# Performance work log

Measured on AMD Instinct MI355X. Metric: run time of the kernel, lower is better.

## Reference

```python
import jax, jax.numpy as jnp
import numpy as np

EMBED = 512
HEADS = 8
HEAD_DIM = EMBED // HEADS


def setup_inputs() -> dict:
    key = jax.random.key(0)
    ks = jax.random.split(key, 12)
    B, L, D = 2, 4096, EMBED
    s = 1.0 / np.sqrt(D)  # torch Linear default init range scale (approx, uniform)
    def lin(k):
        kw, kb = jax.random.split(k)
        W = jax.random.uniform(kw, (D, D), jnp.float32, -s, s)
        b = jax.random.uniform(kb, (D,), jnp.float32, -s, s)
        return W, b
    Wq, bq = lin(ks[0])
    Wk, bk = lin(ks[1])
    Wv, bv = lin(ks[2])
    Wo, bo = lin(ks[3])
    query = jax.random.normal(ks[4], (B, L, D), jnp.float32)
    key_t = jax.random.normal(ks[5], (B, L, D), jnp.float32)
    value = jax.random.normal(ks[6], (B, L, D), jnp.float32)
    return {"query": query, "key": key_t, "value": value,
            "Wq": Wq, "bq": bq, "Wk": Wk, "bk": bk,
            "Wv": Wv, "bv": bv, "Wo": Wo, "bo": bo}


def reference(query, key, value, Wq, bq, Wk, bk, Wv, bv, Wo, bo):
    B, L, D = query.shape
    H, Hd = HEADS, HEAD_DIM
    scale = Hd ** -0.5
    # torch nn.Linear: y = x @ W.T + b
    q = (query @ Wq.T + bq).reshape(B, L, H, Hd).transpose(0, 2, 1, 3)   # [B,H,L,Hd]
    k = (key   @ Wk.T + bk).reshape(B, -1, H, Hd).transpose(0, 2, 1, 3)
    v = (value @ Wv.T + bv).reshape(B, -1, H, Hd).transpose(0, 2, 1, 3)
    scores = jnp.einsum('bhqd,bhkd->bhqk', q, k) * scale                  # [B,H,L,L]
    causal = jnp.triu(jnp.ones((L, L), dtype=bool), k=1)                  # True above diag
    neg = jnp.finfo(scores.dtype).min
    scores = jnp.where(causal, neg, scores)
    attn = jax.nn.softmax(scores, axis=-1)
    # dropout is identity in eval mode
    out = jnp.einsum('bhqk,bhkd->bhqd', attn, v)                          # [B,H,L,Hd]
    out = out.transpose(0, 2, 1, 3).reshape(B, L, D)
    return out @ Wo.T + bo, attn
```

## Files before the change

### kernel.cpp

```cpp
#include <hip/hip_runtime.h>
#include <hip/hip_bf16.h>


typedef __attribute__((ext_vector_type(8))) __bf16 bf16x8;
typedef __attribute__((ext_vector_type(4))) __bf16 bf16v4;
typedef __attribute__((ext_vector_type(4))) float f32x4;

constexpr int LL = 4096;
constexpr int DD = 512;
constexpr int HH = 8;
constexpr int HD = 64;
constexpr int BB = 2;
constexpr int BL = BB * LL;
constexpr size_t OUT_ELEMS = (size_t)BB * LL * DD;
constexpr int CH = 8;
constexpr int NCHUNK = LL / 64 / CH;
constexpr int CHUNKS_PER_BH = 288;

static __device__ inline int chunk_off(int qb) {
    const int g = qb >> 3, r = qb & 7;
    return qb + 4 * g * (g - 1) + r * g;
}

static __device__ inline bf16x8 cvt8(const float* p) {
    float4 a = *reinterpret_cast<const float4*>(p);
    float4 b = *reinterpret_cast<const float4*>(p + 4);
    bf16x8 r;
    r[0] = (__bf16)a.x; r[1] = (__bf16)a.y; r[2] = (__bf16)a.z; r[3] = (__bf16)a.w;
    r[4] = (__bf16)b.x; r[5] = (__bf16)b.y; r[6] = (__bf16)b.z; r[7] = (__bf16)b.w;
    return r;
}

__global__ __launch_bounds__(256) void cvt_kernel(
    const float* __restrict__ q, const float* __restrict__ k,
    const float* __restrict__ v, __bf16* __restrict__ o)
{
    constexpr size_t N = (size_t)BL * DD;
    size_t i = ((size_t)blockIdx.x * 256 + threadIdx.x) * 8;
    const float* src = q; size_t j = i;
    if (i >= 2 * N)      { src = v; j = i - 2 * N; }
    else if (i >= N)     { src = k; j = i - N; }
    *reinterpret_cast<bf16x8*>(&o[i]) = cvt8(&src[j]);
}

__global__ __launch_bounds__(256) void qkv_kernel(
    const __bf16* __restrict__ Xb,
    const float* __restrict__ Wq, const float* __restrict__ bq,
    const float* __restrict__ Wk, const float* __restrict__ bk,
    const float* __restrict__ Wv, const float* __restrict__ bv,
    __bf16* __restrict__ Qb, __bf16* __restrict__ Kb, __bf16* __restrict__ Vt)
{
    const int z = blockIdx.z;
    const __bf16* x  = Xb + (size_t)z * BL * DD;
    const float* W   = (z == 0) ? Wq : (z == 1) ? Wk : Wv;
    const float* bia = (z == 0) ? bq : (z == 1) ? bk : bv;

    const int wid = threadIdx.x >> 6;
    const int lane = threadIdx.x & 63;
    const int l15 = lane & 15;
    const int lg  = lane >> 4;

    const int r0 = blockIdx.x * 64;
    const int cb = blockIdx.y;
    const int c0 = cb * 64 + wid * 16;

    f32x4 acc[4] = {};
    for (int k0 = 0; k0 < DD; k0 += 32) {
        bf16x8 bfrag = cvt8(&W[(size_t)(c0 + l15) * DD + k0 + lg * 8]);
#pragma unroll
        for (int mt = 0; mt < 4; ++mt) {
            bf16x8 afrag = *reinterpret_cast<const bf16x8*>(
                &x[(size_t)(r0 + mt * 16 + l15) * DD + k0 + lg * 8]);
            acc[mt] = __builtin_amdgcn_mfma_f32_16x16x32_bf16(afrag, bfrag, acc[mt], 0, 0, 0);
        }
    }

    __shared__ __bf16 T[64][72];
    const float bval = bia[c0 + l15];
#pragma unroll
    for (int mt = 0; mt < 4; ++mt)
#pragma unroll
        for (int i = 0; i < 4; ++i) {
            const float val = acc[mt][i] + bval;
            const int row = mt * 16 + lg * 4 + i;
            const int col = wid * 16 + l15;
            if (z == 2) T[col][row] = (__bf16)val;
            else        T[row][col] = (__bf16)val;
        }
    __syncthreads();

    const int tr  = threadIdx.x >> 2;
    const int seg = threadIdx.x & 3;
    uint4 v0 = *reinterpret_cast<const uint4*>(&T[tr][seg * 16]);
    uint4 v1 = *reinterpret_cast<const uint4*>(&T[tr][seg * 16 + 8]);
    const int b  = r0 >> 12;
    const int l0 = r0 & (LL - 1);
    if (z == 2) {
        __bf16* dst = Vt + ((size_t)(b * HH + cb) * HD + tr) * LL + l0 + seg * 16;
        *reinterpret_cast<uint4*>(dst)     = v0;
        *reinterpret_cast<uint4*>(dst + 8) = v1;
    } else {
        __bf16* base = (z == 0) ? Qb : Kb;
        __bf16* dst = base + ((size_t)(b * HH + cb) * LL + l0 + tr) * HD + seg * 16;
        *reinterpret_cast<uint4*>(dst)     = v0;
        *reinterpret_cast<uint4*>(dst + 8) = v1;
    }
}

__global__ __launch_bounds__(256, 4) void rowsum_kernel(
    const __bf16* __restrict__ Qb, const __bf16* __restrict__ Kb,
    float* __restrict__ rspart)
{
    const int bh = blockIdx.x;
    const int qb = 63 - blockIdx.y;
    const int ch = blockIdx.z;
    const int kb0 = ch * CH;
    if (kb0 > qb) return;

    const int wv   = threadIdx.x >> 6;
    const int lane = threadIdx.x & 63;
    const int l15  = lane & 15;
    const int lg   = lane >> 4;

    const __bf16* Qh = Qb + (size_t)bh * LL * HD;
    const __bf16* Kh = Kb + (size_t)bh * LL * HD;

    const int q0 = qb * 64 + wv * 16;
    const int qrow = q0 + l15;
    const bf16x8 qf0 = *reinterpret_cast<const bf16x8*>(&Qh[(size_t)qrow * HD + lg * 8]);
    const bf16x8 qf1 = *reinterpret_cast<const bf16x8*>(&Qh[(size_t)qrow * HD + 32 + lg * 8]);
    const float SC = 0.125f * 1.44269504088896f;

    auto loadK = [&](bf16x8 (&kf)[8], int kb) {
        const __bf16* kp = &Kh[((size_t)kb * 64 + l15) * HD + lg * 8];
#pragma unroll
        for (int kt = 0; kt < 4; ++kt) {
            kf[kt * 2]     = *reinterpret_cast<const bf16x8*>(kp + (size_t)kt * 16 * HD);
            kf[kt * 2 + 1] = *reinterpret_cast<const bf16x8*>(kp + (size_t)kt * 16 * HD + 32);
        }
    };

    float rs = 0.f;
    auto body = [&](bf16x8 (&kf)[8], int kb) {
        f32x4 s[4] = {};
#pragma unroll
        for (int kt = 0; kt < 4; ++kt) {
            s[kt] = __builtin_amdgcn_mfma_f32_16x16x32_bf16(kf[kt * 2],     qf0, s[kt], 0, 0, 0);
            s[kt] = __builtin_amdgcn_mfma_f32_16x16x32_bf16(kf[kt * 2 + 1], qf1, s[kt], 0, 0, 0);
        }
        const bool diag = (kb == qb);
#pragma unroll
        for (int kt = 0; kt < 4; ++kt)
#pragma unroll
            for (int i = 0; i < 4; ++i) {
                float e = exp2f(s[kt][i] * SC);
                if (diag && (kb * 64 + kt * 16 + lg * 4 + i) > qrow) e = 0.f;
                rs += e;
            }
    };

    const int kend = (qb < kb0 + CH - 1) ? qb : kb0 + CH - 1;
    {
        bf16x8 kA[8], kB[8];
        int kb = kb0;
        bool useA = true;
        loadK(kA, kb);
        for (; kb <= kend; ++kb) {
            if (useA) { if (kb + 1 <= kend) loadK(kB, kb + 1); body(kA, kb); }
            else      { if (kb + 1 <= kend) loadK(kA, kb + 1); body(kB, kb); }
            useA = !useA;
        }
    }
    rs += __shfl_xor(rs, 16, 64);
    rs += __shfl_xor(rs, 32, 64);
    if (lane < 16)
        rspart[((size_t)bh * LL + qrow) * NCHUNK + ch] = rs;
}

__global__ __launch_bounds__(256, 3) void attn_main_kernel(
    const __bf16* __restrict__ Qb, const __bf16* __restrict__ Kb,
    const __bf16* __restrict__ Vt, const float* __restrict__ rspart,
    __bf16* __restrict__ opart, float* __restrict__ attn_out)
{
    const int bh = blockIdx.x;
    const int qb = 63 - blockIdx.y;
    const int ch = blockIdx.z;

    const int wv   = threadIdx.x >> 6;
    const int lane = threadIdx.x & 63;
    const int l15  = lane & 15;
    const int lg   = lane >> 4;

    float* A_out = attn_out + (size_t)bh * LL * LL;
    const int q0 = qb * 64 + wv * 16;
    const int qrow = q0 + l15;
    const int kb0 = ch * CH;

    const int srow = lane >> 4;
    const int scol = (lane & 15) * 4;

    auto zstore = [&](int kb) {
        const float4 z4 = {0.f, 0.f, 0.f, 0.f};
#pragma unroll
        for (int mt = 0; mt < 4; ++mt)
            *reinterpret_cast<float4*>(
                &A_out[(size_t)(q0 + mt * 4 + srow) * LL + kb * 64 + scol]) = z4;
    };

    if (kb0 > qb) {
        for (int t = 0; t < CH; ++t) zstore(kb0 + t);
        return;
    }

    const __bf16* Qh = Qb + (size_t)bh * LL * HD;
    const __bf16* Kh = Kb + (size_t)bh * LL * HD;
    const __bf16* Vh = Vt + (size_t)bh * HD * LL;

    __shared__ __bf16 P[4][16][72];

    const bf16x8 qf0 = *reinterpret_cast<const bf16x8*>(&Qh[(size_t)qrow * HD + lg * 8]);
    const bf16x8 qf1 = *reinterpret_cast<const bf16x8*>(&Qh[(size_t)qrow * HD + 32 + lg * 8]);

    float rsv = 0.f;
    const int nc = qb >> 3;
    const float* rp = &rspart[((size_t)bh * LL + qrow) * NCHUNK];
    for (int c = 0; c <= nc; ++c) rsv += rp[c];
    const float llog = -log2f(rsv);
    const float SC = 0.125f * 1.44269504088896f;

    f32x4 oacc[4] = {};

    auto loadK = [&](bf16x8 (&kf)[8], int kb) {
        const __bf16* kp = &Kh[((size_t)kb * 64 + l15) * HD + lg * 8];
#pragma unroll
        for (int kt = 0; kt < 4; ++kt) {
            kf[kt * 2]     = *reinterpret_cast<const bf16x8*>(kp + (size_t)kt * 16 * HD);
            kf[kt * 2 + 1] = *reinterpret_cast<const bf16x8*>(kp + (size_t)kt * 16 * HD + 32);
        }
    };

    auto body = [&](bf16x8 (&kf)[8], int kb) {
        bf16x8 vf[8];
        {
            const __bf16* vp = &Vh[(size_t)l15 * LL + (size_t)kb * 64 + lg * 8];
#pragma unroll
            for (int ht = 0; ht < 4; ++ht) {
                vf[ht * 2]     = *reinterpret_cast<const bf16x8*>(vp + (size_t)ht * 16 * LL);
                vf[ht * 2 + 1] = *reinterpret_cast<const bf16x8*>(vp + (size_t)ht * 16 * LL + 32);
            }
        }
        f32x4 s[4] = {};
#pragma unroll
        for (int kt = 0; kt < 4; ++kt) {
            s[kt] = __builtin_amdgcn_mfma_f32_16x16x32_bf16(kf[kt * 2],     qf0, s[kt], 0, 0, 0);
            s[kt] = __builtin_amdgcn_mfma_f32_16x16x32_bf16(kf[kt * 2 + 1], qf1, s[kt], 0, 0, 0);
        }
        const bool diag = (kb == qb);
#pragma unroll
        for (int kt = 0; kt < 4; ++kt) {
            float e0 = exp2f(fmaf(s[kt][0], SC, llog));
            float e1 = exp2f(fmaf(s[kt][1], SC, llog));
            float e2 = exp2f(fmaf(s[kt][2], SC, llog));
            float e3 = exp2f(fmaf(s[kt][3], SC, llog));
            if (diag) {
                const int kc = kb * 64 + kt * 16 + lg * 4;
                if (kc + 0 > qrow) e0 = 0.f;
                if (kc + 1 > qrow) e1 = 0.f;
                if (kc + 2 > qrow) e2 = 0.f;
                if (kc + 3 > qrow) e3 = 0.f;
            }
            float4 ev = {e0, e1, e2, e3};
            *reinterpret_cast<float4*>(
                &A_out[(size_t)qrow * LL + kb * 64 + kt * 16 + lg * 4]) = ev;
            bf16v4 pk;
            pk[0] = (__bf16)e0; pk[1] = (__bf16)e1;
            pk[2] = (__bf16)e2; pk[3] = (__bf16)e3;
            *reinterpret_cast<bf16v4*>(&P[wv][l15][kt * 16 + lg * 4]) = pk;
        }
        const bf16x8 pa0 = *reinterpret_cast<const bf16x8*>(&P[wv][l15][lg * 8]);
        const bf16x8 pa1 = *reinterpret_cast<const bf16x8*>(&P[wv][l15][32 + lg * 8]);
#pragma unroll
        for (int ht = 0; ht < 4; ++ht) {
            oacc[ht] = __builtin_amdgcn_mfma_f32_16x16x32_bf16(pa0, vf[ht * 2],     oacc[ht], 0, 0, 0);
            oacc[ht] = __builtin_amdgcn_mfma_f32_16x16x32_bf16(pa1, vf[ht * 2 + 1], oacc[ht], 0, 0, 0);
        }
    };

    const int kend = (qb < kb0 + CH - 1) ? qb : kb0 + CH - 1;
    {
        bf16x8 kA[8], kB[8];
        int kb = kb0;
        bool useA = true;
        loadK(kA, kb);
        for (; kb <= kend; ++kb) {
            if (useA) { if (kb + 1 <= kend) loadK(kB, kb + 1); body(kA, kb); }
            else      { if (kb + 1 <= kend) loadK(kA, kb + 1); body(kB, kb); }
            useA = !useA;
        }
    }
    for (int kb = qb + 1; kb < kb0 + CH; ++kb) zstore(kb);

#pragma unroll
    for (int ht = 0; ht < 4; ++ht)
#pragma unroll
        for (int i = 0; i < 4; ++i)
            P[wv][lg * 4 + i][ht * 16 + l15] = (__bf16)oacc[ht][i];
    const int arow = lane >> 2;
    const int aseg = lane & 3;
    uint4 o0 = *reinterpret_cast<const uint4*>(&P[wv][arow][aseg * 16]);
    uint4 o1 = *reinterpret_cast<const uint4*>(&P[wv][arow][aseg * 16 + 8]);
    __bf16* dst = opart
        + ((size_t)(bh * CHUNKS_PER_BH + chunk_off(qb) + ch)) * 4096
        + (wv * 16 + arow) * 64 + aseg * 16;
    *reinterpret_cast<uint4*>(dst)     = o0;
    *reinterpret_cast<uint4*>(dst + 8) = o1;
}

__global__ __launch_bounds__(256) void oreduce_kernel(
    const __bf16* __restrict__ opart, __bf16* __restrict__ Ob)
{
    const int bh = blockIdx.x;
    const int qb = blockIdx.y;
    const int nc = qb >> 3;
    const __bf16* src = opart + ((size_t)(bh * CHUNKS_PER_BH + chunk_off(qb))) * 4096;
    const int t = threadIdx.x;

    float acc[16] = {};
    for (int c = 0; c <= nc; ++c) {
        bf16x8 a = *reinterpret_cast<const bf16x8*>(&src[(size_t)c * 4096 + t * 16]);
        bf16x8 b = *reinterpret_cast<const bf16x8*>(&src[(size_t)c * 4096 + t * 16 + 8]);
#pragma unroll
        for (int j = 0; j < 8; ++j) { acc[j] += (float)a[j]; acc[8 + j] += (float)b[j]; }
    }
    bf16x8 r0, r1;
#pragma unroll
    for (int j = 0; j < 8; ++j) { r0[j] = (__bf16)acc[j]; r1[j] = (__bf16)acc[8 + j]; }

    const int qr  = t >> 2;
    const int hd0 = (t & 3) * 16;
    const int b = bh >> 3, h = bh & 7;
    __bf16* dst = Ob + ((size_t)(b * LL + qb * 64 + qr)) * DD + h * HD + hd0;
    *reinterpret_cast<bf16x8*>(dst)     = r0;
    *reinterpret_cast<bf16x8*>(dst + 8) = r1;
}

__global__ __launch_bounds__(256) void oproj_kernel(
    const __bf16* __restrict__ Ob, const float* __restrict__ Wo,
    const float* __restrict__ bo, float* __restrict__ out)
{
    const int wid = threadIdx.x >> 6;
    const int lane = threadIdx.x & 63;
    const int l15 = lane & 15;
    const int lg  = lane >> 4;

    const int r0 = blockIdx.x * 64;
    const int c0 = blockIdx.y * 64 + wid * 16;

    f32x4 acc[4] = {};
    for (int k0 = 0; k0 < DD; k0 += 32) {
        bf16x8 bfrag = cvt8(&Wo[(size_t)(c0 + l15) * DD + k0 + lg * 8]);
#pragma unroll
        for (int mt = 0; mt < 4; ++mt) {
            bf16x8 afrag = *reinterpret_cast<const bf16x8*>(
                &Ob[(size_t)(r0 + mt * 16 + l15) * DD + k0 + lg * 8]);
            acc[mt] = __builtin_amdgcn_mfma_f32_16x16x32_bf16(afrag, bfrag, acc[mt], 0, 0, 0);
        }
    }
    const float bval = bo[c0 + l15];
#pragma unroll
    for (int mt = 0; mt < 4; ++mt)
#pragma unroll
        for (int i = 0; i < 4; ++i)
            out[(size_t)(r0 + mt * 16 + lg * 4 + i) * DD + c0 + l15] = acc[mt][i] + bval;
}

extern "C" void kernel_launch(void* const* d_in, const int* in_sizes, int n_in,
                              void* d_out, int out_size, void* d_ws, size_t ws_size,
                              hipStream_t stream) {
    const float* query = (const float*)d_in[0];
    const float* key_t = (const float*)d_in[1];
    const float* value = (const float*)d_in[2];
    const float* Wq = (const float*)d_in[3];
    const float* bq = (const float*)d_in[4];
    const float* Wk = (const float*)d_in[5];
    const float* bk = (const float*)d_in[6];
    const float* Wv = (const float*)d_in[7];
    const float* bv = (const float*)d_in[8];
    const float* Wo = (const float*)d_in[9];
    const float* bo = (const float*)d_in[10];

    float* out  = (float*)d_out;
    float* attn = out + OUT_ELEMS;

    char* ws = (char*)d_ws;
    __bf16* Qb     = (__bf16*)(ws);
    __bf16* Kb     = (__bf16*)(ws +  8388608);
    __bf16* Vt     = (__bf16*)(ws + 16777216);
    __bf16* Ob     = (__bf16*)(ws + 25165824);
    float*  rspart = (float*) (ws + 33554432);
    __bf16* Xb     = (__bf16*)(ws + 35651584);
    __bf16* opart  = (__bf16*)(ws + 35651584);

    cvt_kernel<<<dim3(3 * BL * DD / 8 / 256), 256, 0, stream>>>(query, key_t, value, Xb);
    qkv_kernel<<<dim3(BL / 64, DD / 64, 3), 256, 0, stream>>>(
        Xb, Wq, bq, Wk, bk, Wv, bv, Qb, Kb, Vt);
    rowsum_kernel<<<dim3(BB * HH, LL / 64, NCHUNK), 256, 0, stream>>>(Qb, Kb, rspart);
    attn_main_kernel<<<dim3(BB * HH, LL / 64, NCHUNK), 256, 0, stream>>>(
        Qb, Kb, Vt, rspart, opart, attn);
    oreduce_kernel<<<dim3(BB * HH, LL / 64), 256, 0, stream>>>(opart, Ob);
    oproj_kernel<<<dim3(BL / 64, DD / 64), 256, 0, stream>>>(Ob, Wo, bo, out);
}
```

Before: 813.2 us.

## Move causal-zero fill to dedicated kernel and coalesce attn stores via LDS

The upper-triangle zero fill of the attention-probability output moves out of the attention kernel into a separate zero_kernel that writes contiguous row strips per query block. In the attention kernel, probabilities are first staged through a shared float tile so each wave writes full 64-float row segments instead of scattered 16-byte pieces. Both changes aim at better-coalesced HBM writes for the large attn tensor. The cost is an extra kernel launch and more shared memory (about 17KB more per block), which may reduce occupancy.

```diff
diff --git a/kernel.cpp b/kernel.cpp
--- a/kernel.cpp
+++ b/kernel.cpp
@@ -41,6 +41,27 @@
     if (i >= 2 * N)      { src = v; j = i - 2 * N; }
     else if (i >= N)     { src = k; j = i - N; }
     *reinterpret_cast<bf16x8*>(&o[i]) = cvt8(&src[j]);
+}
+
+__global__ __launch_bounds__(256) void zero_kernel(float* __restrict__ attn_out)
+{
+    const int bh = blockIdx.x;
+    const int qb = blockIdx.y;
+    const int z  = blockIdx.z;
+
+    const int wv   = threadIdx.x >> 6;
+    const int lane = threadIdx.x & 63;
+
+    const int strip = 1024 - (qb + 1) * 16;
+    const int col0  = (qb + 1) * 64 + z * strip;
+    float* base = attn_out + (size_t)bh * LL * LL + (size_t)qb * 64 * LL;
+
+    const f32x4 z4 = {0.f, 0.f, 0.f, 0.f};
+    for (int r = wv; r < 64; r += 4) {
+        float* row = base + (size_t)r * LL + col0;
+        for (int c = lane * 4; c < strip; c += 256)
+            *reinterpret_cast<f32x4*>(row + c) = z4;
+    }
 }
 
 __global__ __launch_bounds__(256) void qkv_kernel(
@@ -185,6 +206,8 @@
     const int bh = blockIdx.x;
     const int qb = 63 - blockIdx.y;
     const int ch = blockIdx.z;
+    const int kb0 = ch * CH;
+    if (kb0 > qb) return;
 
     const int wv   = threadIdx.x >> 6;
     const int lane = threadIdx.x & 63;
@@ -194,29 +217,13 @@
     float* A_out = attn_out + (size_t)bh * LL * LL;
     const int q0 = qb * 64 + wv * 16;
     const int qrow = q0 + l15;
-    const int kb0 = ch * CH;
-
-    const int srow = lane >> 4;
-    const int scol = (lane & 15) * 4;
-
-    auto zstore = [&](int kb) {
-        const float4 z4 = {0.f, 0.f, 0.f, 0.f};
-#pragma unroll
-        for (int mt = 0; mt < 4; ++mt)
-            *reinterpret_cast<float4*>(
-                &A_out[(size_t)(q0 + mt * 4 + srow) * LL + kb * 64 + scol]) = z4;
-    };
-
-    if (kb0 > qb) {
-        for (int t = 0; t < CH; ++t) zstore(kb0 + t);
-        return;
-    }
 
     const __bf16* Qh = Qb + (size_t)bh * LL * HD;
     const __bf16* Kh = Kb + (size_t)bh * LL * HD;
     const __bf16* Vh = Vt + (size_t)bh * HD * LL;
 
-    __shared__ __bf16 P[4][16][72];
+    __shared__ float  Pf[4][16][68];
+    __shared__ __bf16 Pb[4][16][72];
 
     const bf16x8 qf0 = *reinterpret_cast<const bf16x8*>(&Qh[(size_t)qrow * HD + lg * 8]);
     const bf16x8 qf1 = *reinterpret_cast<const bf16x8*>(&Qh[(size_t)qrow * HD + 32 + lg * 8]);
@@ -229,6 +236,9 @@
     const float SC = 0.125f * 1.44269504088896f;
 
     f32x4 oacc[4] = {};
+
+    const int srow = lane >> 4;
+    const int scol = (lane & 15) * 4;
 
     auto loadK = [&](bf16x8 (&kf)[8], int kb) {
         const __bf16* kp = &Kh[((size_t)kb * 64 + l15) * HD + lg * 8];
@@ -269,16 +279,22 @@
                 if (kc + 2 > qrow) e2 = 0.f;
                 if (kc + 3 > qrow) e3 = 0.f;
             }
-            float4 ev = {e0, e1, e2, e3};
-            *reinterpret_cast<float4*>(
-                &A_out[(size_t)qrow * LL + kb * 64 + kt * 16 + lg * 4]) = ev;
+            f32x4 ev = {e0, e1, e2, e3};
+            *reinterpret_cast<f32x4*>(&Pf[wv][l15][kt * 16 + lg * 4]) = ev;
             bf16v4 pk;
             pk[0] = (__bf16)e0; pk[1] = (__bf16)e1;
             pk[2] = (__bf16)e2; pk[3] = (__bf16)e3;
-            *reinterpret_cast<bf16v4*>(&P[wv][l15][kt * 16 + lg * 4]) = pk;
-        }
-        const bf16x8 pa0 = *reinterpret_cast<const bf16x8*>(&P[wv][l15][lg * 8]);
-        const bf16x8 pa1 = *reinterpret_cast<const bf16x8*>(&P[wv][l15][32 + lg * 8]);
+            *reinterpret_cast<bf16v4*>(&Pb[wv][l15][kt * 16 + lg * 4]) = pk;
+        }
+#pragma unroll
+        for (int rq = 0; rq < 4; ++rq) {
+            const int row = rq * 4 + srow;
+            f32x4 v = *reinterpret_cast<const f32x4*>(&Pf[wv][row][scol]);
+            *reinterpret_cast<f32x4*>(
+                &A_out[(size_t)(q0 + row) * LL + kb * 64 + scol]) = v;
+        }
+        const bf16x8 pa0 = *reinterpret_cast<const bf16x8*>(&Pb[wv][l15][lg * 8]);
+        const bf16x8 pa1 = *reinterpret_cast<const bf16x8*>(&Pb[wv][l15][32 + lg * 8]);
 #pragma unroll
         for (int ht = 0; ht < 4; ++ht) {
             oacc[ht] = __builtin_amdgcn_mfma_f32_16x16x32_bf16(pa0, vf[ht * 2],     oacc[ht], 0, 0, 0);
@@ -298,17 +314,16 @@
             useA = !useA;
         }
     }
-    for (int kb = qb + 1; kb < kb0 + CH; ++kb) zstore(kb);
 
 #pragma unroll
     for (int ht = 0; ht < 4; ++ht)
 #pragma unroll
         for (int i = 0; i < 4; ++i)
-            P[wv][lg * 4 + i][ht * 16 + l15] = (__bf16)oacc[ht][i];
+            Pb[wv][lg * 4 + i][ht * 16 + l15] = (__bf16)oacc[ht][i];
     const int arow = lane >> 2;
     const int aseg = lane & 3;
-    uint4 o0 = *reinterpret_cast<const uint4*>(&P[wv][arow][aseg * 16]);
-    uint4 o1 = *reinterpret_cast<const uint4*>(&P[wv][arow][aseg * 16 + 8]);
+    uint4 o0 = *reinterpret_cast<const uint4*>(&Pb[wv][arow][aseg * 16]);
+    uint4 o1 = *reinterpret_cast<const uint4*>(&Pb[wv][arow][aseg * 16 + 8]);
     __bf16* dst = opart
         + ((size_t)(bh * CHUNKS_PER_BH + chunk_off(qb) + ch)) * 4096
         + (wv * 16 + arow) * 64 + aseg * 16;
@@ -402,6 +417,7 @@
     __bf16* opart  = (__bf16*)(ws + 35651584);
 
     cvt_kernel<<<dim3(3 * BL * DD / 8 / 256), 256, 0, stream>>>(query, key_t, value, Xb);
+    zero_kernel<<<dim3(BB * HH, LL / 64 - 1, 4), 256, 0, stream>>>(attn);
     qkv_kernel<<<dim3(BL / 64, DD / 64, 3), 256, 0, stream>>>(
         Xb, Wq, bq, Wk, bk, Wv, bv, Qb, Kb, Vt);
     rowsum_kernel<<<dim3(BB * HH, LL / 64, NCHUNK), 256, 0, stream>>>(Qb, Kb, rspart);
```

Result: no change. 819.6 us (+0.8%).
